# Kernel tuning notes

Measured on AMD Instinct MI355X. Metric: run time of the kernel, lower is better.

## Reference

```python
import jax, jax.numpy as jnp
import numpy as np

B, T, D = 4, 2048, 1024
H = 4                      # fla GatedLinearAttention default num_heads
K = D; V = D               # expand_k = expand_v = 1
DK = K // H; DV = V // H   # 256 each
LOW = 16                   # gate_low_rank_dim default
GLN = 16.0                 # gate_logit_normalizer default


def _layernorm(x, w, b, eps=1e-5):
    mu = x.mean(-1, keepdims=True)
    xc = x - mu
    var = (xc * xc).mean(-1, keepdims=True)
    return xc * jax.lax.rsqrt(var + eps) * w + b


def _rmsnorm(x, w, eps=1e-5):
    ms = (x * x).mean(-1, keepdims=True)
    return x * jax.lax.rsqrt(ms + eps) * w


def _gla_scan(q, k, v, gk):
    # q,k,gk: [B,T,H,DK]; v: [B,T,H,DV]
    scale = DK ** -0.5
    qT = jnp.moveaxis(q * scale, 1, 0)  # [T,B,H,DK]
    kT = jnp.moveaxis(k, 1, 0)
    vT = jnp.moveaxis(v, 1, 0)
    gT = jnp.moveaxis(gk, 1, 0)

    def step(h, inp):
        qt, kt, vt, gt = inp  # [B,H,DK]/[B,H,DV]
        h = h * jnp.exp(gt)[..., None] + kt[..., :, None] * vt[..., None, :]
        o = jnp.einsum('bhk,bhkv->bhv', qt, h)
        return h, o

    h0 = jnp.zeros((q.shape[0], H, DK, DV), q.dtype)
    _, oT = jax.lax.scan(step, h0, (qT, kT, vT, gT))
    return jnp.moveaxis(oT, 0, 1)  # [B,T,H,DV]


def setup_inputs() -> dict:
    key = jax.random.key(0)
    ks = jax.random.split(key, 12)
    rn = lambda k, s: jax.random.normal(k, s, jnp.float32) * 0.02
    return {
        'x': jax.random.normal(ks[0], (B, T, D), jnp.float32),
        'ln1_w': jnp.ones((D,), jnp.float32), 'ln1_b': jnp.zeros((D,), jnp.float32),
        'Wq': rn(ks[1], (D, K)), 'Wk': rn(ks[2], (D, K)), 'Wv': rn(ks[3], (D, V)),
        'Wg': rn(ks[4], (D, V)),
        'Wgk1': rn(ks[5], (D, LOW)), 'Wgk2': rn(ks[6], (LOW, K)), 'bgk2': jnp.zeros((K,), jnp.float32),
        'rms_w': jnp.ones((DV,), jnp.float32),
        'Wo': rn(ks[7], (V, D)),
        'ln2_w': jnp.ones((D,), jnp.float32), 'ln2_b': jnp.zeros((D,), jnp.float32),
        'W1': rn(ks[8], (D, 3 * D)), 'b1': jnp.zeros((3 * D,), jnp.float32),
        'W2': rn(ks[9], (3 * D, D)), 'b2': jnp.zeros((D,), jnp.float32),
    }


def reference(x, ln1_w, ln1_b, Wq, Wk, Wv, Wg, Wgk1, Wgk2, bgk2, rms_w, Wo,
              ln2_w, ln2_b, W1, b1, W2, b2):
    b, t = x.shape[0], x.shape[1]
    xn = _layernorm(x, ln1_w, ln1_b)
    q = (xn @ Wq).reshape(b, t, H, DK)
    k = (xn @ Wk).reshape(b, t, H, DK)
    v = (xn @ Wv).reshape(b, t, H, DV)
    # low-rank forget gate: logsigmoid / gate_logit_normalizer
    gk = (jax.nn.log_sigmoid((xn @ Wgk1) @ Wgk2 + bgk2) / GLN).reshape(b, t, H, DK)
    o = _gla_scan(q, k, v, gk)                      # [B,T,H,DV]
    g = (xn @ Wg).reshape(b, t, H, DV)              # output gate
    o = _rmsnorm(o, rms_w) * (g * jax.nn.sigmoid(g))  # gated RMSNorm (swish gate)
    o = o.reshape(b, t, V) @ Wo
    x = x + o
    xn2 = _layernorm(x, ln2_w, ln2_b)
    h = jax.nn.leaky_relu(xn2 @ W1 + b1, 0.01)
    h = h * h                                        # LeakyReLU^2
    x = x + (h @ W2 + b2)
    return x
```

## Files before the change

kernel.cpp:

```cpp
#include <hip/hip_runtime.h>
#include <math.h>

#define BB 4
#define TT 2048
#define DD 1024
#define HH 4
#define DK 256
#define DV 256
#define RR 8192
#define CHK 64
#define NCHK 32
#define SS ((size_t)RR * DD)

typedef __bf16 bf16x8 __attribute__((ext_vector_type(8)));
typedef float f32x4 __attribute__((ext_vector_type(4)));

static __device__ inline unsigned short f2bf(float f) {
  unsigned int u = __float_as_uint(f);
  unsigned int r = (u + 0x7fffu + ((u >> 16) & 1u)) >> 16;
  return (unsigned short)r;
}
static __device__ inline float bf2f(unsigned short h) {
  return __uint_as_float(((unsigned int)h) << 16);
}

static __device__ __forceinline__ void gload16(const unsigned short* g,
                                               unsigned short* l) {
  __builtin_amdgcn_global_load_lds(
      (const __attribute__((address_space(1))) void*)g,
      (__attribute__((address_space(3))) void*)l, 16, 0, 0);
}

__global__ __launch_bounds__(256) void ln_kernel(const float* __restrict__ x,
                                                 const float* __restrict__ w,
                                                 const float* __restrict__ b,
                                                 unsigned short* __restrict__ yb) {
  int row = blockIdx.x;
  const float* xr = x + (size_t)row * DD;
  unsigned short* ybr = yb + (size_t)row * DD;
  int tid = threadIdx.x;

  float4 v = ((const float4*)xr)[tid];
  float s = v.x + v.y + v.z + v.w;
  float ss = v.x * v.x + v.y * v.y + v.z * v.z + v.w * v.w;
#pragma unroll
  for (int o = 32; o > 0; o >>= 1) {
    s += __shfl_down(s, o);
    ss += __shfl_down(ss, o);
  }
  __shared__ float ls[4], lss[4];
  int wid = tid >> 6;
  if ((tid & 63) == 0) { ls[wid] = s; lss[wid] = ss; }
  __syncthreads();
  float sum = ls[0] + ls[1] + ls[2] + ls[3];
  float sumsq = lss[0] + lss[1] + lss[2] + lss[3];
  float mu = sum * (1.0f / DD);
  float var = sumsq * (1.0f / DD) - mu * mu;
  float rs = rsqrtf(var + 1e-5f);

  float4 wv = ((const float4*)w)[tid];
  float4 bv = ((const float4*)b)[tid];
  ushort4 ob;
  ob.x = f2bf((v.x - mu) * rs * wv.x + bv.x);
  ob.y = f2bf((v.y - mu) * rs * wv.y + bv.y);
  ob.z = f2bf((v.z - mu) * rs * wv.z + bv.z);
  ob.w = f2bf((v.w - mu) * rs * wv.w + bv.w);
  ((ushort4*)ybr)[tid] = ob;
}

__global__ __launch_bounds__(256) void transpose_cast(const float* __restrict__ W,
                                                      unsigned short* __restrict__ Wt,
                                                      int K, int N) {
  __shared__ float t[32][33];
  int k0 = blockIdx.y * 32, n0 = blockIdx.x * 32;
  int tid = threadIdx.x;
  int tx = tid & 31, ty = tid >> 5;
#pragma unroll
  for (int i = 0; i < 4; ++i)
    t[ty + i * 8][tx] = W[(size_t)(k0 + ty + i * 8) * N + n0 + tx];
  __syncthreads();
#pragma unroll
  for (int i = 0; i < 4; ++i)
    Wt[(size_t)(n0 + ty + i * 8) * K + k0 + tx] = f2bf(t[tx][ty + i * 8]);
}

struct P5 {
  const float* w[5];
  unsigned short* o[5];
};
__global__ __launch_bounds__(256) void transpose5(P5 p) {
  __shared__ float t[32][33];
  int z = blockIdx.z;
  const float* W = p.w[z];
  unsigned short* Wt = p.o[z];
  int k0 = blockIdx.y * 32, n0 = blockIdx.x * 32;
  int tid = threadIdx.x;
  int tx = tid & 31, ty = tid >> 5;
#pragma unroll
  for (int i = 0; i < 4; ++i)
    t[ty + i * 8][tx] = W[(size_t)(k0 + ty + i * 8) * 1024 + n0 + tx];
  __syncthreads();
#pragma unroll
  for (int i = 0; i < 4; ++i)
    Wt[(size_t)(n0 + ty + i * 8) * 1024 + k0 + tx] = f2bf(t[tx][ty + i * 8]);
}

template <int EPI, int OUTBF>
__global__ __launch_bounds__(256) void gemm_bf16(
    const unsigned short* __restrict__ A,
    const unsigned short* __restrict__ Bt,
    const float* __restrict__ bias, const float* __restrict__ Res,
    void* __restrict__ Cv, int M, int N, int K) {
  __shared__ unsigned short As[2][128 * 64];
  __shared__ unsigned short Bs[2][128 * 64];
  int tid = threadIdx.x;
  int nwg = gridDim.x * gridDim.y;
  int wg = blockIdx.y * gridDim.x + blockIdx.x;
  int cpx = nwg >> 3;
  wg = (wg & 7) * cpx + (wg >> 3);
  int m0 = (wg / gridDim.x) * 128, n0 = (wg % gridDim.x) * 128;
  int lane = tid & 63;
  int w64 = tid & 192;
  int wid = tid >> 6;
  int wm = (wid >> 1) * 64, wn = (wid & 1) * 64;
  int fr = lane & 15, fq = lane >> 4;

  f32x4 acc[4][4] = {};

  auto STAGE = [&](int buf, int k0) {
#pragma unroll
    for (int j = 0; j < 4; ++j) {
      int gl = j * 256 + tid;
      int row = gl >> 3;
      int gs = (gl & 7) ^ (row & 7);
      gload16(&A[(size_t)(m0 + row) * K + k0 + gs * 8],
              &As[buf][(size_t)(j * 256 + w64) * 8]);
      gload16(&Bt[(size_t)(n0 + row) * K + k0 + gs * 8],
              &Bs[buf][(size_t)(j * 256 + w64) * 8]);
    }
  };

  STAGE(0, 0);
  asm volatile("s_waitcnt vmcnt(0)");
  __syncthreads();

  int cur = 0;
  for (int k0 = 0; k0 < K; k0 += 64) {
    if (k0 + 64 < K) STAGE(cur ^ 1, k0 + 64);

#pragma unroll
    for (int ph = 0; ph < 2; ++ph) {
      bf16x8 af[4], bv[4];
#pragma unroll
      for (int i = 0; i < 4; ++i) {
        int ra = wm + i * 16 + fr;
        af[i] = *(const bf16x8*)&As[cur][ra * 64 + (((ph * 4 + fq) ^ (ra & 7)) * 8)];
        int rb = wn + i * 16 + fr;
        bv[i] = *(const bf16x8*)&Bs[cur][rb * 64 + (((ph * 4 + fq) ^ (rb & 7)) * 8)];
      }
#pragma unroll
      for (int i = 0; i < 4; ++i)
#pragma unroll
        for (int jj = 0; jj < 4; ++jj)
          acc[i][jj] = __builtin_amdgcn_mfma_f32_16x16x32_bf16(af[i], bv[jj],
                                                               acc[i][jj], 0, 0, 0);
    }
    __syncthreads();
    cur ^= 1;
  }

  int col = lane & 15;
  int rbase = (lane >> 4) * 4;
#pragma unroll
  for (int i = 0; i < 4; ++i) {
#pragma unroll
    for (int j = 0; j < 4; ++j) {
      int n = n0 + wn + j * 16 + col;
      float bvv = (EPI == 2 || EPI == 4) ? bias[n] : 0.0f;
#pragma unroll
      for (int r = 0; r < 4; ++r) {
        int m = m0 + wm + i * 16 + rbase + r;
        float vv = acc[i][j][r] + bvv;
        if (EPI == 2) {
          float t = vv > 0.0f ? vv : 0.01f * vv;
          vv = t * t;
        }
        if (EPI == 3 || EPI == 4) vv += Res[(size_t)m * N + n];
        if (EPI == 5) {
          ((unsigned short*)Cv)[(size_t)(n >> 10) * SS + (size_t)m * 1024 +
                                (n & 1023)] = f2bf(vv);
        } else if (OUTBF) {
          ((unsigned short*)Cv)[(size_t)m * N + n] = f2bf(vv);
        } else {
          ((float*)Cv)[(size_t)m * N + n] = vv;
        }
      }
    }
  }
}

__global__ __launch_bounds__(256) void gk_kernel(const unsigned short* __restrict__ xn,
                                                 const float* __restrict__ Wgk1,
                                                 const float* __restrict__ Wgk2,
                                                 const float* __restrict__ bgk2,
                                                 unsigned short* __restrict__ gk) {
  __shared__ unsigned short Xs[16 * 1024];
  __shared__ unsigned short W1s[1024 * 16];
  __shared__ float Ts[16][16];
  int r0 = blockIdx.x * 16;
  int tid = threadIdx.x;

#pragma unroll
  for (int i = 0; i < 16; ++i) {
    int idx = tid + i * 256;
    ((ushort4*)Xs)[idx] = ((const ushort4*)(xn + (size_t)r0 * 1024))[idx];
  }
#pragma unroll
  for (int i = 0; i < 16; ++i) {
    int idx = tid + i * 256;
    float4 w = ((const float4*)Wgk1)[idx];
    ushort4 hh;
    hh.x = f2bf(w.x); hh.y = f2bf(w.y); hh.z = f2bf(w.z); hh.w = f2bf(w.w);
    ((ushort4*)W1s)[idx] = hh;
  }
  __syncthreads();

  {
    int r = tid >> 4, part = tid & 15;
    float t16[16];
#pragma unroll
    for (int j = 0; j < 16; ++j) t16[j] = 0.0f;
    for (int dd = 0; dd < 64; ++dd) {
      int d = dd * 16 + part;
      float xv = bf2f(Xs[r * 1024 + d]);
      const ushort4* wr = (const ushort4*)&W1s[d * 16];
#pragma unroll
      for (int q4 = 0; q4 < 4; ++q4) {
        ushort4 w = wr[q4];
        t16[q4 * 4 + 0] += xv * bf2f(w.x);
        t16[q4 * 4 + 1] += xv * bf2f(w.y);
        t16[q4 * 4 + 2] += xv * bf2f(w.z);
        t16[q4 * 4 + 3] += xv * bf2f(w.w);
      }
    }
#pragma unroll
    for (int j = 0; j < 16; ++j) {
      float s = t16[j];
      s += __shfl_xor(s, 1);
      s += __shfl_xor(s, 2);
      s += __shfl_xor(s, 4);
      s += __shfl_xor(s, 8);
      t16[j] = s;
    }
    if (part == 0) {
#pragma unroll
      for (int j = 0; j < 16; ++j) Ts[r][j] = t16[j];
    }
  }
  __syncthreads();

  {
    float w2[16][4];
#pragma unroll
    for (int j = 0; j < 16; ++j) {
      float4 wv = *(const float4*)&Wgk2[(size_t)j * 1024 + tid * 4];
      w2[j][0] = wv.x; w2[j][1] = wv.y; w2[j][2] = wv.z; w2[j][3] = wv.w;
    }
    float4 bv = *(const float4*)&bgk2[tid * 4];
    float bb[4] = {bv.x, bv.y, bv.z, bv.w};
#pragma unroll
    for (int r = 0; r < 16; ++r) {
      ushort4 outv;
      unsigned short* op = (unsigned short*)&outv;
#pragma unroll
      for (int jj = 0; jj < 4; ++jj) {
        float z = bb[jj];
#pragma unroll
        for (int j = 0; j < 16; ++j) z += Ts[r][j] * w2[j][jj];
        float lsg = fminf(z, 0.0f) - log1pf(expf(-fabsf(z)));
        op[jj] = f2bf(lsg * (1.0f / 16.0f));
      }
      *(ushort4*)&Xs[r * 1024 + tid * 4] = outv;
    }
  }
  __syncthreads();
#pragma unroll
  for (int i = 0; i < 16; ++i) {
    int idx = tid + i * 256;
    ((ushort4*)(gk + (size_t)r0 * 1024))[idx] = ((const ushort4*)Xs)[idx];
  }
}

__global__ __launch_bounds__(256) void gate_chunk(const unsigned short* __restrict__ gk,
                                                  unsigned short* __restrict__ q,
                                                  unsigned short* __restrict__ k,
                                                  float* __restrict__ ebC) {
  int bid = blockIdx.x;
  int c = bid & 31;
  int h = (bid >> 5) & 3;
  int b = bid >> 7;
  int tid = threadIdx.x;
  size_t base = ((size_t)b * TT + c * CHK) * 1024 + h * 256 + tid;

  float cums[64];
#pragma unroll
  for (int t = 0; t < 64; ++t) cums[t] = bf2f(gk[base + (size_t)t * 1024]);
  float cum = 0.0f;
#pragma unroll
  for (int t = 0; t < 64; ++t) {
    cum += cums[t];
    cums[t] = cum;
  }
  ebC[((b * 4 + h) * NCHK + c) * 256 + tid] = expf(cum);

  const float scale = 0.0625f;
#pragma unroll
  for (int t = 0; t < 64; ++t) {
    size_t a = base + (size_t)t * 1024;
    q[a] = f2bf(bf2f(q[a]) * expf(cums[t]) * scale);
    k[a] = f2bf(bf2f(k[a]) * expf(-cums[t]));
  }
}

__global__ __launch_bounds__(256) void trans2(const unsigned short* __restrict__ kin,
                                              const unsigned short* __restrict__ vin,
                                              const float* __restrict__ ebC,
                                              unsigned short* __restrict__ kout,
                                              unsigned short* __restrict__ vout) {
  __shared__ unsigned short T[64][68];
  int bid0 = blockIdx.x;
  int mode = bid0 >> 11;
  int bid = bid0 & 2047;
  const unsigned short* in = mode ? vin : kin;
  unsigned short* outT = mode ? vout : kout;
  int dkt = bid & 3;
  int ct = (bid >> 2) & 31;
  int bh = bid >> 7;
  int b = bh >> 2, h = bh & 3;
  int tid = threadIdx.x;
  int r = tid >> 4;
  int c4 = (tid & 15) * 4;
  size_t srcbase = ((size_t)b * TT + ct * 64) * 1024 + h * 256 + dkt * 64;
#pragma unroll
  for (int i = 0; i < 4; ++i)
    *(ushort4*)&T[r + i * 16][c4] =
        *(const ushort4*)&in[srcbase + (size_t)(r + i * 16) * 1024 + c4];
  __syncthreads();
  size_t outbase = (size_t)bh * 524288 + (size_t)(dkt * 64) * 2048 + ct * 64;
  const float* ep = ebC + ((size_t)bh * 32 + ct) * 256 + dkt * 64;
#pragma unroll
  for (int i = 0; i < 4; ++i) {
    int dkl = r + i * 16;
    float e = mode ? 1.0f : ep[dkl];
    ushort4 o;
    o.x = f2bf(bf2f(T[c4 + 0][dkl]) * e);
    o.y = f2bf(bf2f(T[c4 + 1][dkl]) * e);
    o.z = f2bf(bf2f(T[c4 + 2][dkl]) * e);
    o.w = f2bf(bf2f(T[c4 + 3][dkl]) * e);
    *(ushort4*)&outT[outbase + (size_t)dkl * 2048 + c4] = o;
  }
}

__global__ __launch_bounds__(256) void ustate_kernel(
    const unsigned short* __restrict__ khatT, const unsigned short* __restrict__ vT,
    const float* __restrict__ ebC, unsigned short* __restrict__ HT) {
  __shared__ unsigned short Vs[2][64 * 72];
  __shared__ unsigned short Ks[2][64 * 72];
  int bid = blockIdx.x;
  int tile = bid & 15;
  int bh = bid >> 4;
  int dv0 = (tile >> 2) * 64, dk0 = (tile & 3) * 64;
  const unsigned short* Vb = vT + (size_t)bh * 524288 + (size_t)dv0 * 2048;
  const unsigned short* Kb = khatT + (size_t)bh * 524288 + (size_t)dk0 * 2048;
  int tid = threadIdx.x;
  int lane = tid & 63;
  int w = tid >> 6;
  int fr = lane & 15, fq = lane >> 4;

  bf16x8 vr[2], kr[2], nvr[2], nkr[2];
  auto LOADR = [&](int c, bf16x8 vv[2], bf16x8 kk[2]) {
#pragma unroll
    for (int j = 0; j < 2; ++j) {
      int g = j * 256 + tid;
      int row = g >> 3, gc = g & 7;
      vv[j] = *(const bf16x8*)&Vb[(size_t)row * 2048 + c * 64 + gc * 8];
      kk[j] = *(const bf16x8*)&Kb[(size_t)row * 2048 + c * 64 + gc * 8];
    }
  };
  auto WLDS = [&](int buf, bf16x8 vv[2], bf16x8 kk[2]) {
#pragma unroll
    for (int j = 0; j < 2; ++j) {
      int g = j * 256 + tid;
      int row = g >> 3, gc = g & 7;
      *(bf16x8*)&Vs[buf][row * 72 + gc * 8] = vv[j];
      *(bf16x8*)&Ks[buf][row * 72 + gc * 8] = kk[j];
    }
  };

  f32x4 st[4] = {};

  LOADR(0, vr, kr);
  WLDS(0, vr, kr);
  __syncthreads();

  for (int c = 0; c < NCHK; ++c) {
    int cur = c & 1;
    if (c + 1 < NCHK) LOADR(c + 1, nvr, nkr);

    size_t hb = ((size_t)(bh * NCHK + c)) * 65536;
#pragma unroll
    for (int nj = 0; nj < 4; ++nj) {
#pragma unroll
      for (int r = 0; r < 4; ++r) {
        int dv = dv0 + w * 16 + fq * 4 + r;
        int dk = dk0 + nj * 16 + fr;
        HT[hb + (size_t)dv * 256 + dk] = f2bf(st[nj][r]);
      }
    }

    f32x4 uacc[4] = {};
#pragma unroll
    for (int ks = 0; ks < 2; ++ks) {
      bf16x8 av = *(const bf16x8*)&Vs[cur][(w * 16 + fr) * 72 + ks * 32 + fq * 8];
#pragma unroll
      for (int nj = 0; nj < 4; ++nj) {
        bf16x8 bk = *(const bf16x8*)&Ks[cur][(nj * 16 + fr) * 72 + ks * 32 + fq * 8];
        uacc[nj] = __builtin_amdgcn_mfma_f32_16x16x32_bf16(av, bk, uacc[nj], 0, 0, 0);
      }
    }

    const float* ec = ebC + ((size_t)bh * NCHK + c) * 256 + dk0;
#pragma unroll
    for (int nj = 0; nj < 4; ++nj) {
      float e = ec[nj * 16 + fr];
      st[nj] = e * st[nj] + uacc[nj];
    }

    __syncthreads();
    if (c + 1 < NCHK) {
      WLDS(cur ^ 1, nvr, nkr);
      __syncthreads();
    }
  }
}

__global__ __launch_bounds__(256) void attn_fused(
    const unsigned short* __restrict__ qt, const unsigned short* __restrict__ kt,
    const unsigned short* __restrict__ vT, const unsigned short* __restrict__ HT,
    const unsigned short* __restrict__ gp, const float* __restrict__ rw,
    unsigned short* __restrict__ og) {
  __shared__ unsigned short Qs[64 * 264];
  __shared__ unsigned short KVH[256 * 72];
  __shared__ unsigned short Sb[64 * 64];
  __shared__ float red[64][4];

  int bid = blockIdx.x;
  int c = bid & 31;
  int bh = bid >> 5;
  int b = bh >> 2, h = bh & 3;
  size_t rowbase = ((size_t)b * TT + c * 64) * 1024 + h * 256;
  size_t vtbase = (size_t)bh * 524288 + c * 64;
  size_t htbase = ((size_t)(bh * 32 + c)) * 65536;
  int tid = threadIdx.x;
  int lane = tid & 63;
  int w = tid >> 6;
  int fr = lane & 15, fq = lane >> 4;

#pragma unroll
  for (int i = 0; i < 8; ++i) {
    int gg = tid + i * 256;
    int row = gg >> 5, gc = gg & 31;
    *(bf16x8*)&Qs[row * 264 + gc * 8] =
        *(const bf16x8*)&qt[rowbase + (size_t)row * 1024 + gc * 8];
    *(bf16x8*)&KVH[row * 264 + gc * 8] =
        *(const bf16x8*)&kt[rowbase + (size_t)row * 1024 + gc * 8];
  }
  __syncthreads();

  {
    f32x4 accs[4] = {};
#pragma unroll
    for (int ks = 0; ks < 8; ++ks) {
      bf16x8 af = *(const bf16x8*)&Qs[(w * 16 + fr) * 264 + ks * 32 + fq * 8];
#pragma unroll
      for (int si = 0; si < 4; ++si) {
        bf16x8 bf_ = *(const bf16x8*)&KVH[(si * 16 + fr) * 264 + ks * 32 + fq * 8];
        accs[si] = __builtin_amdgcn_mfma_f32_16x16x32_bf16(af, bf_, accs[si], 0, 0, 0);
      }
    }
#pragma unroll
    for (int si = 0; si < 4; ++si) {
#pragma unroll
      for (int r = 0; r < 4; ++r) {
        int t = w * 16 + fq * 4 + r;
        int s = si * 16 + fr;
        float val = (s <= t) ? accs[si][r] : 0.0f;
        Sb[t * 64 + (((s >> 3) ^ (t & 7)) * 8) + (s & 7)] = f2bf(val);
      }
    }
  }
  __syncthreads();

#pragma unroll
  for (int i = 0; i < 8; ++i) {
    int gg = tid + i * 256;
    int dv = gg >> 3, gc = gg & 7;
    *(bf16x8*)&KVH[dv * 72 + gc * 8] =
        *(const bf16x8*)&vT[vtbase + (size_t)dv * 2048 + gc * 8];
  }
  __syncthreads();

  int dv0 = w * 64;
  f32x4 acc[4][4] = {};

#pragma unroll
  for (int ks = 0; ks < 2; ++ks) {
    bf16x8 af[4], bv[4];
#pragma unroll
    for (int ti = 0; ti < 4; ++ti) {
      int t = ti * 16 + fr;
      af[ti] = *(const bf16x8*)&Sb[t * 64 + (((ks * 4 + fq) ^ (t & 7)) * 8)];
    }
#pragma unroll
    for (int nj = 0; nj < 4; ++nj)
      bv[nj] = *(const bf16x8*)&KVH[(dv0 + nj * 16 + fr) * 72 + ks * 32 + fq * 8];
#pragma unroll
    for (int ti = 0; ti < 4; ++ti)
#pragma unroll
      for (int nj = 0; nj < 4; ++nj)
        acc[ti][nj] = __builtin_amdgcn_mfma_f32_16x16x32_bf16(af[ti], bv[nj],
                                                              acc[ti][nj], 0, 0, 0);
  }

  for (int k4 = 0; k4 < 4; ++k4) {
    __syncthreads();
#pragma unroll
    for (int i = 0; i < 8; ++i) {
      int gg = tid + i * 256;
      int dv = gg >> 3, gc = gg & 7;
      *(bf16x8*)&KVH[dv * 72 + gc * 8] =
          *(const bf16x8*)&HT[htbase + (size_t)dv * 256 + k4 * 64 + gc * 8];
    }
    __syncthreads();
#pragma unroll
    for (int ks = 0; ks < 2; ++ks) {
      bf16x8 af[4], bv[4];
#pragma unroll
      for (int ti = 0; ti < 4; ++ti)
        af[ti] = *(const bf16x8*)&Qs[(ti * 16 + fr) * 264 + k4 * 64 + ks * 32 + fq * 8];
#pragma unroll
      for (int nj = 0; nj < 4; ++nj)
        bv[nj] = *(const bf16x8*)&KVH[(dv0 + nj * 16 + fr) * 72 + ks * 32 + fq * 8];
#pragma unroll
      for (int ti = 0; ti < 4; ++ti)
#pragma unroll
        for (int nj = 0; nj < 4; ++nj)
          acc[ti][nj] = __builtin_amdgcn_mfma_f32_16x16x32_bf16(af[ti], bv[nj],
                                                                acc[ti][nj], 0, 0, 0);
    }
  }

  float rstd[4][4];
#pragma unroll
  for (int ti = 0; ti < 4; ++ti) {
#pragma unroll
    for (int r = 0; r < 4; ++r) {
      float s = 0.0f;
#pragma unroll
      for (int nj = 0; nj < 4; ++nj) {
        float v = acc[ti][nj][r];
        s += v * v;
      }
      s += __shfl_xor(s, 1);
      s += __shfl_xor(s, 2);
      s += __shfl_xor(s, 4);
      s += __shfl_xor(s, 8);
      rstd[ti][r] = s;
    }
  }
  if (fr == 0) {
#pragma unroll
    for (int ti = 0; ti < 4; ++ti)
#pragma unroll
      for (int r = 0; r < 4; ++r)
        red[ti * 16 + fq * 4 + r][w] = rstd[ti][r];
  }
  __syncthreads();
#pragma unroll
  for (int ti = 0; ti < 4; ++ti) {
#pragma unroll
    for (int r = 0; r < 4; ++r) {
      int t = ti * 16 + fq * 4 + r;
      float tot = red[t][0] + red[t][1] + red[t][2] + red[t][3];
      rstd[ti][r] = rsqrtf(tot * (1.0f / 256.0f) + 1e-5f);
    }
  }
#pragma unroll
  for (int ti = 0; ti < 4; ++ti) {
#pragma unroll
    for (int nj = 0; nj < 4; ++nj) {
      int dv = dv0 + nj * 16 + fr;
      float rwv = rw[dv];
#pragma unroll
      for (int r = 0; r < 4; ++r) {
        int t = ti * 16 + fq * 4 + r;
        float gv = bf2f(gp[rowbase + (size_t)t * 1024 + dv]);
        float sw = gv / (1.0f + expf(-gv));
        og[rowbase + (size_t)t * 1024 + dv] =
            f2bf(acc[ti][nj][r] * rstd[ti][r] * rwv * sw);
      }
    }
  }
}

extern "C" void kernel_launch(void* const* d_in, const int* in_sizes, int n_in,
                              void* d_out, int out_size, void* d_ws,
                              size_t ws_size, hipStream_t stream) {
  const float* x = (const float*)d_in[0];
  const float* ln1_w = (const float*)d_in[1];
  const float* ln1_b = (const float*)d_in[2];
  const float* Wq = (const float*)d_in[3];
  const float* Wk = (const float*)d_in[4];
  const float* Wv = (const float*)d_in[5];
  const float* Wg = (const float*)d_in[6];
  const float* Wgk1 = (const float*)d_in[7];
  const float* Wgk2 = (const float*)d_in[8];
  const float* bgk2 = (const float*)d_in[9];
  const float* rms_w = (const float*)d_in[10];
  const float* Wo = (const float*)d_in[11];
  const float* ln2_w = (const float*)d_in[12];
  const float* ln2_b = (const float*)d_in[13];
  const float* W1 = (const float*)d_in[14];
  const float* b1 = (const float*)d_in[15];
  const float* W2 = (const float*)d_in[16];
  const float* b2 = (const float*)d_in[17];
  float* out = (float*)d_out;

  const size_t S = SS;
  unsigned short* actb = (unsigned short*)d_ws;
  unsigned short* qb = actb + S;
  unsigned short* kb = qb + S;
  unsigned short* vb = kb + S;
  unsigned short* gb = vb + S;
  unsigned short* gkb = gb + S;
  unsigned short* ogb = gkb + S;
  unsigned short* UH = ogb + 2 * S;
  float* ebC = (float*)(UH + 4 * S);
  unsigned short* Wqkvgt = (unsigned short*)(ebC + 131072);
  unsigned short* Wot = Wqkvgt + 4194304;
  unsigned short* W1t = Wot + 1048576;
  unsigned short* W2t = W1t + 3145728;
  unsigned short* khatT = gkb;
  unsigned short* vT = actb;
  float* x1 = (float*)kb;
  unsigned short* hb = UH;

  dim3 blk(256);

  P5 p5;
  p5.w[0] = Wq;  p5.o[0] = Wqkvgt;
  p5.w[1] = Wk;  p5.o[1] = Wqkvgt + 1048576;
  p5.w[2] = Wv;  p5.o[2] = Wqkvgt + 2097152;
  p5.w[3] = Wg;  p5.o[3] = Wqkvgt + 3145728;
  p5.w[4] = Wo;  p5.o[4] = Wot;
  transpose5<<<dim3(32, 32, 5), blk, 0, stream>>>(p5);
  transpose_cast<<<dim3(96, 32), blk, 0, stream>>>(W1, W1t, 1024, 3072);
  transpose_cast<<<dim3(32, 96), blk, 0, stream>>>(W2, W2t, 3072, 1024);

  ln_kernel<<<RR, blk, 0, stream>>>(x, ln1_w, ln1_b, actb);

  dim3 g4096(4096 / 128, RR / 128);
  gemm_bf16<5, 1><<<g4096, blk, 0, stream>>>(actb, Wqkvgt, nullptr, nullptr, qb,
                                             RR, 4096, 1024);

  gk_kernel<<<RR / 16, blk, 0, stream>>>(actb, Wgk1, Wgk2, bgk2, gkb);

  gate_chunk<<<BB * HH * NCHK, blk, 0, stream>>>(gkb, qb, kb, ebC);

  trans2<<<2 * 16 * 32 * 4, blk, 0, stream>>>(kb, vb, ebC, khatT, vT);

  ustate_kernel<<<16 * 16, blk, 0, stream>>>(khatT, vT, ebC, UH);

  attn_fused<<<16 * NCHK, blk, 0, stream>>>(qb, kb, vT, UH, gb, rms_w, ogb);

  dim3 g1024(1024 / 128, RR / 128);
  gemm_bf16<3, 0><<<g1024, blk, 0, stream>>>(ogb, Wot, nullptr, x, x1, RR, 1024, 1024);

  ln_kernel<<<RR, blk, 0, stream>>>(x1, ln2_w, ln2_b, actb);

  dim3 g3072(3072 / 128, RR / 128);
  gemm_bf16<2, 1><<<g3072, blk, 0, stream>>>(actb, W1t, b1, nullptr, hb, RR, 3072, 1024);

  gemm_bf16<4, 0><<<g1024, blk, 0, stream>>>(hb, W2t, b2, x1, out, RR, 1024, 3072);
}
```

Measured before the change: 412.1 us.

## Fuse gate cumsum with k/v transposes and store residual x1 in bf16

Merges the per-chunk gate cumulative-sum kernel and the k/v transpose kernel into one kernel. It does the chunk scan through shared memory with a parallel prefix over four groups and writes the gated k directly into the transposed layout, so gk, k and v are not re-read across two launches. Separately, the attention output projection now writes the residual stream x1 in bf16 instead of fp32, and the following LayerNorm and final GEMM epilogue read it as bf16. This halves x1 traffic but adds rounding error to the residual path. The khatT buffer moves to a different workspace slot so it no longer overlaps gk.

```diff
diff --git a/kernel.cpp b/kernel.cpp
--- a/kernel.cpp
+++ b/kernel.cpp
@@ -31,18 +31,27 @@
       (__attribute__((address_space(3))) void*)l, 16, 0, 0);
 }
 
-__global__ __launch_bounds__(256) void ln_kernel(const float* __restrict__ x,
+template <int INBF>
+__global__ __launch_bounds__(256) void ln_kernel(const void* __restrict__ xv,
                                                  const float* __restrict__ w,
                                                  const float* __restrict__ b,
                                                  unsigned short* __restrict__ yb) {
   int row = blockIdx.x;
-  const float* xr = x + (size_t)row * DD;
+  int tid = threadIdx.x;
   unsigned short* ybr = yb + (size_t)row * DD;
-  int tid = threadIdx.x;
-
-  float4 v = ((const float4*)xr)[tid];
-  float s = v.x + v.y + v.z + v.w;
-  float ss = v.x * v.x + v.y * v.y + v.z * v.z + v.w * v.w;
+
+  float e0, e1, e2, e3;
+  if (INBF) {
+    const unsigned short* xr = (const unsigned short*)xv + (size_t)row * DD;
+    ushort4 u = ((const ushort4*)xr)[tid];
+    e0 = bf2f(u.x); e1 = bf2f(u.y); e2 = bf2f(u.z); e3 = bf2f(u.w);
+  } else {
+    const float* xr = (const float*)xv + (size_t)row * DD;
+    float4 v = ((const float4*)xr)[tid];
+    e0 = v.x; e1 = v.y; e2 = v.z; e3 = v.w;
+  }
+  float s = e0 + e1 + e2 + e3;
+  float ss = e0 * e0 + e1 * e1 + e2 * e2 + e3 * e3;
 #pragma unroll
   for (int o = 32; o > 0; o >>= 1) {
     s += __shfl_down(s, o);
@@ -61,10 +70,10 @@
   float4 wv = ((const float4*)w)[tid];
   float4 bv = ((const float4*)b)[tid];
   ushort4 ob;
-  ob.x = f2bf((v.x - mu) * rs * wv.x + bv.x);
-  ob.y = f2bf((v.y - mu) * rs * wv.y + bv.y);
-  ob.z = f2bf((v.z - mu) * rs * wv.z + bv.z);
-  ob.w = f2bf((v.w - mu) * rs * wv.w + bv.w);
+  ob.x = f2bf((e0 - mu) * rs * wv.x + bv.x);
+  ob.y = f2bf((e1 - mu) * rs * wv.y + bv.y);
+  ob.z = f2bf((e2 - mu) * rs * wv.z + bv.z);
+  ob.w = f2bf((e3 - mu) * rs * wv.w + bv.w);
   ((ushort4*)ybr)[tid] = ob;
 }
 
@@ -109,7 +118,7 @@
 __global__ __launch_bounds__(256) void gemm_bf16(
     const unsigned short* __restrict__ A,
     const unsigned short* __restrict__ Bt,
-    const float* __restrict__ bias, const float* __restrict__ Res,
+    const float* __restrict__ bias, const void* __restrict__ Res,
     void* __restrict__ Cv, int M, int N, int K) {
   __shared__ unsigned short As[2][128 * 64];
   __shared__ unsigned short Bs[2][128 * 64];
@@ -176,7 +185,7 @@
 #pragma unroll
     for (int j = 0; j < 4; ++j) {
       int n = n0 + wn + j * 16 + col;
-      float bvv = (EPI == 2 || EPI == 4) ? bias[n] : 0.0f;
+      float bvv = (EPI == 2 || EPI == 4 || EPI == 6) ? bias[n] : 0.0f;
 #pragma unroll
       for (int r = 0; r < 4; ++r) {
         int m = m0 + wm + i * 16 + rbase + r;
@@ -185,7 +194,10 @@
           float t = vv > 0.0f ? vv : 0.01f * vv;
           vv = t * t;
         }
-        if (EPI == 3 || EPI == 4) vv += Res[(size_t)m * N + n];
+        if (EPI == 3 || EPI == 4)
+          vv += ((const float*)Res)[(size_t)m * N + n];
+        if (EPI == 6)
+          vv += bf2f(((const unsigned short*)Res)[(size_t)m * N + n]);
         if (EPI == 5) {
           ((unsigned short*)Cv)[(size_t)(n >> 10) * SS + (size_t)m * 1024 +
                                 (n & 1023)] = f2bf(vv);
@@ -291,73 +303,118 @@
   }
 }
 
-__global__ __launch_bounds__(256) void gate_chunk(const unsigned short* __restrict__ gk,
-                                                  unsigned short* __restrict__ q,
-                                                  unsigned short* __restrict__ k,
-                                                  float* __restrict__ ebC) {
+__global__ __launch_bounds__(256) void gate_trans(
+    const unsigned short* __restrict__ gk, unsigned short* __restrict__ q,
+    unsigned short* __restrict__ k, const unsigned short* __restrict__ v,
+    float* __restrict__ ebC, unsigned short* __restrict__ khatT,
+    unsigned short* __restrict__ vT) {
+  __shared__ float Gs[64][65];
+  __shared__ unsigned short T[64][68];
+  __shared__ float P[4][64];
+  __shared__ float E[64];
   int bid = blockIdx.x;
-  int c = bid & 31;
-  int h = (bid >> 5) & 3;
-  int b = bid >> 7;
-  int tid = threadIdx.x;
-  size_t base = ((size_t)b * TT + c * CHK) * 1024 + h * 256 + tid;
-
-  float cums[64];
-#pragma unroll
-  for (int t = 0; t < 64; ++t) cums[t] = bf2f(gk[base + (size_t)t * 1024]);
-  float cum = 0.0f;
-#pragma unroll
-  for (int t = 0; t < 64; ++t) {
-    cum += cums[t];
-    cums[t] = cum;
-  }
-  ebC[((b * 4 + h) * NCHK + c) * 256 + tid] = expf(cum);
-
-  const float scale = 0.0625f;
-#pragma unroll
-  for (int t = 0; t < 64; ++t) {
-    size_t a = base + (size_t)t * 1024;
-    q[a] = f2bf(bf2f(q[a]) * expf(cums[t]) * scale);
-    k[a] = f2bf(bf2f(k[a]) * expf(-cums[t]));
-  }
-}
-
-__global__ __launch_bounds__(256) void trans2(const unsigned short* __restrict__ kin,
-                                              const unsigned short* __restrict__ vin,
-                                              const float* __restrict__ ebC,
-                                              unsigned short* __restrict__ kout,
-                                              unsigned short* __restrict__ vout) {
-  __shared__ unsigned short T[64][68];
-  int bid0 = blockIdx.x;
-  int mode = bid0 >> 11;
-  int bid = bid0 & 2047;
-  const unsigned short* in = mode ? vin : kin;
-  unsigned short* outT = mode ? vout : kout;
-  int dkt = bid & 3;
+  int dt = bid & 3;
   int ct = (bid >> 2) & 31;
   int bh = bid >> 7;
   int b = bh >> 2, h = bh & 3;
   int tid = threadIdx.x;
   int r = tid >> 4;
   int c4 = (tid & 15) * 4;
-  size_t srcbase = ((size_t)b * TT + ct * 64) * 1024 + h * 256 + dkt * 64;
-#pragma unroll
-  for (int i = 0; i < 4; ++i)
-    *(ushort4*)&T[r + i * 16][c4] =
-        *(const ushort4*)&in[srcbase + (size_t)(r + i * 16) * 1024 + c4];
-  __syncthreads();
-  size_t outbase = (size_t)bh * 524288 + (size_t)(dkt * 64) * 2048 + ct * 64;
-  const float* ep = ebC + ((size_t)bh * 32 + ct) * 256 + dkt * 64;
+  size_t srcbase = ((size_t)b * TT + ct * 64) * 1024 + h * 256 + dt * 64;
+  size_t outbase = (size_t)bh * 524288 + (size_t)(dt * 64) * 2048 + ct * 64;
+
+#pragma unroll
+  for (int i = 0; i < 4; ++i) {
+    ushort4 g4 = *(const ushort4*)&gk[srcbase + (size_t)(r + i * 16) * 1024 + c4];
+    Gs[r + i * 16][c4 + 0] = bf2f(g4.x);
+    Gs[r + i * 16][c4 + 1] = bf2f(g4.y);
+    Gs[r + i * 16][c4 + 2] = bf2f(g4.z);
+    Gs[r + i * 16][c4 + 3] = bf2f(g4.w);
+  }
+  __syncthreads();
+
+  {
+    int col = tid & 63, grp = tid >> 6;
+    float s = 0.0f;
+#pragma unroll
+    for (int t = 0; t < 16; ++t) s += Gs[grp * 16 + t][col];
+    P[grp][col] = s;
+  }
+  __syncthreads();
+  {
+    int col = tid & 63, grp = tid >> 6;
+    float base = 0.0f;
+#pragma unroll
+    for (int j = 0; j < 4; ++j)
+      if (j < grp) base += P[j][col];
+    float cum = base;
+#pragma unroll
+    for (int t = 0; t < 16; ++t) {
+      cum += Gs[grp * 16 + t][col];
+      Gs[grp * 16 + t][col] = cum;
+    }
+    if (grp == 3) {
+      float ebv = expf(cum);
+      E[col] = ebv;
+      ebC[((size_t)bh * NCHK + ct) * 256 + dt * 64 + col] = ebv;
+    }
+  }
+  __syncthreads();
+
+  const float scale = 0.0625f;
+#pragma unroll
+  for (int i = 0; i < 4; ++i) {
+    int t = r + i * 16;
+    size_t a = srcbase + (size_t)t * 1024 + c4;
+    ushort4 q4 = *(const ushort4*)&q[a];
+    ushort4 o;
+    o.x = f2bf(bf2f(q4.x) * expf(Gs[t][c4 + 0]) * scale);
+    o.y = f2bf(bf2f(q4.y) * expf(Gs[t][c4 + 1]) * scale);
+    o.z = f2bf(bf2f(q4.z) * expf(Gs[t][c4 + 2]) * scale);
+    o.w = f2bf(bf2f(q4.w) * expf(Gs[t][c4 + 3]) * scale);
+    *(ushort4*)&q[a] = o;
+  }
+
+#pragma unroll
+  for (int i = 0; i < 4; ++i) {
+    int t = r + i * 16;
+    size_t a = srcbase + (size_t)t * 1024 + c4;
+    ushort4 k4 = *(const ushort4*)&k[a];
+    ushort4 o;
+    o.x = f2bf(bf2f(k4.x) * expf(-Gs[t][c4 + 0]));
+    o.y = f2bf(bf2f(k4.y) * expf(-Gs[t][c4 + 1]));
+    o.z = f2bf(bf2f(k4.z) * expf(-Gs[t][c4 + 2]));
+    o.w = f2bf(bf2f(k4.w) * expf(-Gs[t][c4 + 3]));
+    *(ushort4*)&k[a] = o;
+    *(ushort4*)&T[t][c4] = o;
+  }
+  __syncthreads();
 #pragma unroll
   for (int i = 0; i < 4; ++i) {
     int dkl = r + i * 16;
-    float e = mode ? 1.0f : ep[dkl];
+    float e = E[dkl];
     ushort4 o;
     o.x = f2bf(bf2f(T[c4 + 0][dkl]) * e);
     o.y = f2bf(bf2f(T[c4 + 1][dkl]) * e);
     o.z = f2bf(bf2f(T[c4 + 2][dkl]) * e);
     o.w = f2bf(bf2f(T[c4 + 3][dkl]) * e);
-    *(ushort4*)&outT[outbase + (size_t)dkl * 2048 + c4] = o;
+    *(ushort4*)&khatT[outbase + (size_t)dkl * 2048 + c4] = o;
+  }
+  __syncthreads();
+#pragma unroll
+  for (int i = 0; i < 4; ++i)
+    *(ushort4*)&T[r + i * 16][c4] =
+        *(const ushort4*)&v[srcbase + (size_t)(r + i * 16) * 1024 + c4];
+  __syncthreads();
+#pragma unroll
+  for (int i = 0; i < 4; ++i) {
+    int dvl = r + i * 16;
+    ushort4 o;
+    o.x = T[c4 + 0][dvl];
+    o.y = T[c4 + 1][dvl];
+    o.z = T[c4 + 2][dvl];
+    o.w = T[c4 + 3][dvl];
+    *(ushort4*)&vT[outbase + (size_t)dvl * 2048 + c4] = o;
   }
 }
 
@@ -650,9 +707,9 @@
   unsigned short* Wot = Wqkvgt + 4194304;
   unsigned short* W1t = Wot + 1048576;
   unsigned short* W2t = W1t + 3145728;
-  unsigned short* khatT = gkb;
+  unsigned short* khatT = ogb + S;
   unsigned short* vT = actb;
-  float* x1 = (float*)kb;
+  unsigned short* x1 = kb;
   unsigned short* hb = UH;
 
   dim3 blk(256);
@@ -667,7 +724,7 @@
   transpose_cast<<<dim3(96, 32), blk, 0, stream>>>(W1, W1t, 1024, 3072);
   transpose_cast<<<dim3(32, 96), blk, 0, stream>>>(W2, W2t, 3072, 1024);
 
-  ln_kernel<<<RR, blk, 0, stream>>>(x, ln1_w, ln1_b, actb);
+  ln_kernel<0><<<RR, blk, 0, stream>>>(x, ln1_w, ln1_b, actb);
 
   dim3 g4096(4096 / 128, RR / 128);
   gemm_bf16<5, 1><<<g4096, blk, 0, stream>>>(actb, Wqkvgt, nullptr, nullptr, qb,
@@ -675,21 +732,19 @@
 
   gk_kernel<<<RR / 16, blk, 0, stream>>>(actb, Wgk1, Wgk2, bgk2, gkb);
 
-  gate_chunk<<<BB * HH * NCHK, blk, 0, stream>>>(gkb, qb, kb, ebC);
-
-  trans2<<<2 * 16 * 32 * 4, blk, 0, stream>>>(kb, vb, ebC, khatT, vT);
+  gate_trans<<<16 * 32 * 4, blk, 0, stream>>>(gkb, qb, kb, vb, ebC, khatT, vT);
 
   ustate_kernel<<<16 * 16, blk, 0, stream>>>(khatT, vT, ebC, UH);
 
   attn_fused<<<16 * NCHK, blk, 0, stream>>>(qb, kb, vT, UH, gb, rms_w, ogb);
 
   dim3 g1024(1024 / 128, RR / 128);
-  gemm_bf16<3, 0><<<g1024, blk, 0, stream>>>(ogb, Wot, nullptr, x, x1, RR, 1024, 1024);
-
-  ln_kernel<<<RR, blk, 0, stream>>>(x1, ln2_w, ln2_b, actb);
+  gemm_bf16<3, 1><<<g1024, blk, 0, stream>>>(ogb, Wot, nullptr, x, x1, RR, 1024, 1024);
+
+  ln_kernel<1><<<RR, blk, 0, stream>>>(x1, ln2_w, ln2_b, actb);
 
   dim3 g3072(3072 / 128, RR / 128);
   gemm_bf16<2, 1><<<g3072, blk, 0, stream>>>(actb, W1t, b1, nullptr, hb, RR, 3072, 1024);
 
-  gemm_bf16<4, 0><<<g1024, blk, 0, stream>>>(hb, W2t, b2, x1, out, RR, 1024, 3072);
-}
+  gemm_bf16<6, 0><<<g1024, blk, 0, stream>>>(hb, W2t, b2, x1, out, RR, 1024, 3072);
+}
```

Result: faster. 399.0 us, median of 2 (-3.2%).
